# Kernel optimization log

Hardware: AMD Instinct MI355X
Metric: run time of the kernel (lower is better)

## Reference

```python
import jax, jax.numpy as jnp
import numpy as np

B, N, D, H = 2, 512, 64, 128  # batch, tokens, feature dim, hidden (=2*D)
OUT = 64


def setup_inputs() -> dict:
    key = jax.random.key(0)
    ks = jax.random.split(key, 11)
    sH = 1.0 / np.sqrt(H)
    inp = {
        "x": jax.random.normal(ks[0], (B, N, D), dtype=jnp.float32),
        # inner MLP: Linear(2D->H), ReLU, Linear(H->H), ReLU, Linear(H->H)
        "W1": jax.random.normal(ks[1], (2 * D, H), dtype=jnp.float32) / np.sqrt(2 * D),
        "b1": jnp.zeros((H,), jnp.float32),
        "W2": jax.random.normal(ks[2], (H, H), dtype=jnp.float32) * sH,
        "b2": jnp.zeros((H,), jnp.float32),
        "W3": jax.random.normal(ks[3], (H, H), dtype=jnp.float32) * sH,
        "b3": jnp.zeros((H,), jnp.float32),
        # outer MLP: Linear(H->H), ReLU, Linear(H->OUT)
        "V1": jax.random.normal(ks[4], (H, H), dtype=jnp.float32) * sH,
        "c1": jnp.zeros((H,), jnp.float32),
        "V2": jax.random.normal(ks[5], (H, OUT), dtype=jnp.float32) * sH,
        "c2": jnp.zeros((OUT,), jnp.float32),
    }
    return inp


def reference(x, W1, b1, W2, b2, W3, b3, V1, c1, V2, c2):
    d = x.shape[-1]
    # pair[b,i,j] = cat(x[b,j], x[b,i]); fuse cat with first linear:
    # pair @ W1 = x[b,j] @ W1[:d] + x[b,i] @ W1[d:]
    xa = jnp.einsum('bnd,dh->bnh', x, W1[:d])   # contribution of pair_a (index j)
    xb = jnp.einsum('bnd,dh->bnh', x, W1[d:])   # contribution of pair_b (index i)
    h = jax.nn.relu(xa[:, None, :, :] + xb[:, :, None, :] + b1)  # [B,N,N,H]
    h = jax.nn.relu(jnp.einsum('bijh,hk->bijk', h, W2) + b2)
    rel = jnp.einsum('bijh,hk->bijk', h, W3) + b3                # inner output [B,N,N,H]
    pooled = rel.sum(axis=(1, 2))                                # [B,H]
    o = jax.nn.relu(pooled @ V1 + c1)
    return o @ V2 + c2                                           # [B,OUT]
```

## Files before the change

### kernel.cpp

```cpp
#include <hip/hip_runtime.h>
#include <hip/hip_bf16.h>

#define B_ 2
#define N_ 512
#define D_ 64
#define H_ 128
#define OUT_ 64

using bf16x8 = __attribute__((ext_vector_type(8))) __bf16;
using f32x4  = __attribute__((ext_vector_type(4))) float;


__global__ __launch_bounds__(256) void prep_kernel(
    const float* __restrict__ x, const float* __restrict__ W1,
    const float* __restrict__ b1, const float* __restrict__ W2,
    float* __restrict__ xa, float* __restrict__ xb,
    __hip_bfloat16* __restrict__ w2t, float* __restrict__ S)
{
    int idx = blockIdx.x * 256 + threadIdx.x;
    if (idx < B_ * N_ * H_) {
        int h  = idx & (H_ - 1);
        int bn = idx >> 7;
        const float* xr = x + bn * D_;
        float aa = 0.f, ab = 0.f;
        #pragma unroll
        for (int k = 0; k < D_; k++) {
            float xv = xr[k];
            aa += xv * W1[k * H_ + h];
            ab += xv * W1[(k + D_) * H_ + h];
        }
        xa[idx] = aa + b1[h];
        xb[idx] = ab;
    }
    if (idx < H_ * H_) {
        int k = idx & (H_ - 1);
        int n = idx >> 7;
        w2t[n * H_ + k] = __float2bfloat16(W2[k * H_ + n]);
    }
    if (idx < B_ * H_) S[idx] = 0.f;
}

__global__ __launch_bounds__(256, 2) void pair_kernel(
    const float* __restrict__ xa, const float* __restrict__ xb,
    const uint4* __restrict__ w2t, const float* __restrict__ b2,
    float* __restrict__ S)
{
    const int tid  = threadIdx.x;
    const int lane = tid & 63;
    const int wid  = tid >> 6;
    const int l15  = lane & 15;
    const int quad = lane >> 4;

    const int j0 = blockIdx.x * 16;
    const int i0 = blockIdx.y * 64;
    const int b  = blockIdx.z;

    bf16x8 bfrag[8][4];
    #pragma unroll
    for (int c = 0; c < 8; c++) {
        int row = 16 * c + l15;
        #pragma unroll
        for (int s = 0; s < 4; s++) {
            union { uint4 u; bf16x8 v; } cv;
            cv.u = w2t[row * 16 + s * 4 + quad];
            bfrag[c][s] = cv.v;
        }
    }

    const float* xaB = xa + (size_t)(b * N_ + j0 + l15) * H_;
    f32x4 av[4][2];
    #pragma unroll
    for (int s = 0; s < 4; s++) {
        const f32x4* p = (const f32x4*)(xaB + s * 32 + quad * 8);
        av[s][0] = p[0];
        av[s][1] = p[1];
    }

    float b2v[8];
    #pragma unroll
    for (int c = 0; c < 8; c++) b2v[c] = b2[16 * c + l15];

    float csum[8];
    #pragma unroll
    for (int c = 0; c < 8; c++) csum[c] = 0.f;

    const float* xbB = xb + (size_t)(b * N_) * H_;

    for (int r = 0; r < 16; r++) {
        const int i = i0 + wid * 16 + r;
        const float* xr = xbB + i * H_;

        bf16x8 afr[4];
        #pragma unroll
        for (int s = 0; s < 4; s++) {
            const f32x4* p = (const f32x4*)(xr + s * 32 + quad * 8);
            f32x4 u0 = p[0], u1 = p[1];
            f32x4 v0 = av[s][0], v1 = av[s][1];
            bf16x8 a;
            #pragma unroll
            for (int t = 0; t < 4; t++) {
                float f0 = v0[t] + u0[t]; f0 = f0 > 0.f ? f0 : 0.f;
                float f1 = v1[t] + u1[t]; f1 = f1 > 0.f ? f1 : 0.f;
                a[t]     = (__bf16)f0;
                a[t + 4] = (__bf16)f1;
            }
            afr[s] = a;
        }

        #pragma unroll
        for (int c = 0; c < 8; c++) {
            f32x4 acc = {0.f, 0.f, 0.f, 0.f};
            #pragma unroll
            for (int s = 0; s < 4; s++)
                acc = __builtin_amdgcn_mfma_f32_16x16x32_bf16(afr[s], bfrag[c][s], acc, 0, 0, 0);
            float t0 = acc[0] + b2v[c]; t0 = t0 > 0.f ? t0 : 0.f;
            float t1 = acc[1] + b2v[c]; t1 = t1 > 0.f ? t1 : 0.f;
            float t2 = acc[2] + b2v[c]; t2 = t2 > 0.f ? t2 : 0.f;
            float t3 = acc[3] + b2v[c]; t3 = t3 > 0.f ? t3 : 0.f;
            csum[c] += t0 + t1 + t2 + t3;
        }
    }

    #pragma unroll
    for (int c = 0; c < 8; c++) {
        float v = csum[c];
        v += __shfl_xor(v, 16, 64);
        v += __shfl_xor(v, 32, 64);
        csum[c] = v;
    }

    __shared__ float sred[4][H_];
    if (lane < 16) {
        #pragma unroll
        for (int c = 0; c < 8; c++) sred[wid][c * 16 + l15] = csum[c];
    }
    __syncthreads();
    if (tid < H_) {
        float tot = sred[0][tid] + sred[1][tid] + sred[2][tid] + sred[3][tid];
        atomicAdd(&S[b * H_ + tid], tot);
    }
}

__global__ __launch_bounds__(128) void tail_kernel(
    const float* __restrict__ S, const float* __restrict__ W3,
    const float* __restrict__ b3, const float* __restrict__ V1,
    const float* __restrict__ c1, const float* __restrict__ V2,
    const float* __restrict__ c2, float* __restrict__ out)
{
    __shared__ float pool[H_], ov[H_];
    const int b = blockIdx.x, t = threadIdx.x;
    const float* Sb = S + b * H_;
    float acc = 0.f;
    for (int k = 0; k < H_; k++) acc += Sb[k] * W3[k * H_ + t];
    pool[t] = acc + (float)(N_ * N_) * b3[t];
    __syncthreads();
    acc = c1[t];
    for (int k = 0; k < H_; k++) acc += pool[k] * V1[k * H_ + t];
    ov[t] = acc > 0.f ? acc : 0.f;
    __syncthreads();
    if (t < OUT_) {
        acc = c2[t];
        for (int k = 0; k < H_; k++) acc += ov[k] * V2[k * OUT_ + t];
        out[b * OUT_ + t] = acc;
    }
}

extern "C" void kernel_launch(void* const* d_in, const int* in_sizes, int n_in,
                              void* d_out, int out_size, void* d_ws, size_t ws_size,
                              hipStream_t stream) {
    const float* x  = (const float*)d_in[0];
    const float* W1 = (const float*)d_in[1];
    const float* b1 = (const float*)d_in[2];
    const float* W2 = (const float*)d_in[3];
    const float* b2 = (const float*)d_in[4];
    const float* W3 = (const float*)d_in[5];
    const float* b3 = (const float*)d_in[6];
    const float* V1 = (const float*)d_in[7];
    const float* c1 = (const float*)d_in[8];
    const float* V2 = (const float*)d_in[9];
    const float* c2 = (const float*)d_in[10];
    float* out = (float*)d_out;

    char* ws = (char*)d_ws;
    float*          xa  = (float*)(ws);
    float*          xb  = (float*)(ws + 524288);
    __hip_bfloat16* w2t = (__hip_bfloat16*)(ws + 1048576);
    float*          S   = (float*)(ws + 1048576 + 32768);

    prep_kernel<<<512, 256, 0, stream>>>(x, W1, b1, W2, xa, xb, w2t, S);
    dim3 g2(N_ / 16, N_ / 64, B_);
    pair_kernel<<<g2, 256, 0, stream>>>(xa, xb, (const uint4*)w2t, b2, S);
    tail_kernel<<<B_, 128, 0, stream>>>(S, W3, b3, V1, c1, V2, c2, out);
}
```

Measured before the change: 119.8 us.

## Restructure prep with shared-memory x, double pair grid, vectorize pair inner loop

The prep kernel now stages two x rows per block in shared memory and uses split accumulators, and folds the W2 transpose into 32 threads per block. The pair kernel processes 32 rows of i per block instead of 64, doubling the grid so more CUs are busy, and it fully unrolls the row loop. The add/ReLU/bf16 conversion and the bias/ReLU accumulation are vectorised, which defers the per-lane reduction. Doubling the grid also doubles the per-block reloads of W2 fragments and xa, and doubles the atomic adds.

```diff
diff --git a/kernel.cpp b/kernel.cpp
--- a/kernel.cpp
+++ b/kernel.cpp
@@ -9,6 +9,7 @@
 
 using bf16x8 = __attribute__((ext_vector_type(8))) __bf16;
 using f32x4  = __attribute__((ext_vector_type(4))) float;
+using f32x8  = __attribute__((ext_vector_type(8))) float;
 
 
 __global__ __launch_bounds__(256) void prep_kernel(
@@ -17,27 +18,35 @@
     float* __restrict__ xa, float* __restrict__ xb,
     __hip_bfloat16* __restrict__ w2t, float* __restrict__ S)
 {
-    int idx = blockIdx.x * 256 + threadIdx.x;
-    if (idx < B_ * N_ * H_) {
-        int h  = idx & (H_ - 1);
-        int bn = idx >> 7;
-        const float* xr = x + bn * D_;
-        float aa = 0.f, ab = 0.f;
-        #pragma unroll
-        for (int k = 0; k < D_; k++) {
-            float xv = xr[k];
-            aa += xv * W1[k * H_ + h];
-            ab += xv * W1[(k + D_) * H_ + h];
-        }
-        xa[idx] = aa + b1[h];
-        xb[idx] = ab;
-    }
-    if (idx < H_ * H_) {
-        int k = idx & (H_ - 1);
-        int n = idx >> 7;
+    const int tid = threadIdx.x;
+    const int blk = blockIdx.x;
+    __shared__ float xs[128];
+    if (tid < 128) xs[tid] = x[blk * 128 + tid];
+    if (tid < 32) {
+        int e = blk * 32 + tid;
+        int k = e & (H_ - 1), n = e >> 7;
         w2t[n * H_ + k] = __float2bfloat16(W2[k * H_ + n]);
     }
-    if (idx < B_ * H_) S[idx] = 0.f;
+    if (blk == 0) S[tid] = 0.f;
+    __syncthreads();
+
+    const int h = tid & (H_ - 1);
+    const int which = tid >> 7;
+    const float* xr = xs + which * D_;
+    const float* Wa = W1 + h;
+    const float* Wb = W1 + D_ * H_ + h;
+    float a0 = 0.f, a1 = 0.f, p0 = 0.f, p1 = 0.f;
+    #pragma unroll 8
+    for (int k = 0; k < D_; k += 2) {
+        float x0 = xr[k], x1 = xr[k + 1];
+        a0 += x0 * Wa[k * H_];
+        a1 += x1 * Wa[(k + 1) * H_];
+        p0 += x0 * Wb[k * H_];
+        p1 += x1 * Wb[(k + 1) * H_];
+    }
+    const int bn = blk * 2 + which;
+    xa[bn * H_ + h] = a0 + a1 + b1[h];
+    xb[bn * H_ + h] = p0 + p1;
 }
 
 __global__ __launch_bounds__(256, 2) void pair_kernel(
@@ -52,7 +61,7 @@
     const int quad = lane >> 4;
 
     const int j0 = blockIdx.x * 16;
-    const int i0 = blockIdx.y * 64;
+    const int i0 = blockIdx.y * 32;
     const int b  = blockIdx.z;
 
     bf16x8 bfrag[8][4];
@@ -67,72 +76,51 @@
         }
     }
 
-    const float* xaB = xa + (size_t)(b * N_ + j0 + l15) * H_;
-    f32x4 av[4][2];
+    const float* xaB = xa + (size_t)(b * N_ + j0 + l15) * H_ + quad * 8;
+    f32x8 av[4];
     #pragma unroll
-    for (int s = 0; s < 4; s++) {
-        const f32x4* p = (const f32x4*)(xaB + s * 32 + quad * 8);
-        av[s][0] = p[0];
-        av[s][1] = p[1];
-    }
+    for (int s = 0; s < 4; s++) av[s] = *(const f32x8*)(xaB + s * 32);
 
-    float b2v[8];
+    float b2s[8];
     #pragma unroll
-    for (int c = 0; c < 8; c++) b2v[c] = b2[16 * c + l15];
+    for (int c = 0; c < 8; c++) b2s[c] = b2[16 * c + l15];
 
-    float csum[8];
+    f32x4 csum[8];
     #pragma unroll
-    for (int c = 0; c < 8; c++) csum[c] = 0.f;
+    for (int c = 0; c < 8; c++) csum[c] = (f32x4)0.f;
 
-    const float* xbB = xb + (size_t)(b * N_) * H_;
+    const float* xbB = xb + (size_t)(b * N_ + i0 + wid * 8) * H_ + quad * 8;
 
-    for (int r = 0; r < 16; r++) {
-        const int i = i0 + wid * 16 + r;
-        const float* xr = xbB + i * H_;
-
+    #pragma unroll
+    for (int r = 0; r < 8; r++) {
+        const float* xr = xbB + r * H_;
         bf16x8 afr[4];
         #pragma unroll
         for (int s = 0; s < 4; s++) {
-            const f32x4* p = (const f32x4*)(xr + s * 32 + quad * 8);
-            f32x4 u0 = p[0], u1 = p[1];
-            f32x4 v0 = av[s][0], v1 = av[s][1];
-            bf16x8 a;
-            #pragma unroll
-            for (int t = 0; t < 4; t++) {
-                float f0 = v0[t] + u0[t]; f0 = f0 > 0.f ? f0 : 0.f;
-                float f1 = v1[t] + u1[t]; f1 = f1 > 0.f ? f1 : 0.f;
-                a[t]     = (__bf16)f0;
-                a[t + 4] = (__bf16)f1;
-            }
-            afr[s] = a;
+            f32x8 u = *(const f32x8*)(xr + s * 32);
+            f32x8 v = av[s] + u;
+            v = __builtin_elementwise_max(v, (f32x8)0.f);
+            afr[s] = __builtin_convertvector(v, bf16x8);
         }
-
         #pragma unroll
         for (int c = 0; c < 8; c++) {
-            f32x4 acc = {0.f, 0.f, 0.f, 0.f};
+            f32x4 acc = (f32x4)0.f;
             #pragma unroll
             for (int s = 0; s < 4; s++)
                 acc = __builtin_amdgcn_mfma_f32_16x16x32_bf16(afr[s], bfrag[c][s], acc, 0, 0, 0);
-            float t0 = acc[0] + b2v[c]; t0 = t0 > 0.f ? t0 : 0.f;
-            float t1 = acc[1] + b2v[c]; t1 = t1 > 0.f ? t1 : 0.f;
-            float t2 = acc[2] + b2v[c]; t2 = t2 > 0.f ? t2 : 0.f;
-            float t3 = acc[3] + b2v[c]; t3 = t3 > 0.f ? t3 : 0.f;
-            csum[c] += t0 + t1 + t2 + t3;
+            f32x4 t = acc + b2s[c];
+            t = __builtin_elementwise_max(t, (f32x4)0.f);
+            csum[c] += t;
         }
     }
 
+    __shared__ float sred[4][H_];
     #pragma unroll
     for (int c = 0; c < 8; c++) {
-        float v = csum[c];
+        float v = (csum[c][0] + csum[c][1]) + (csum[c][2] + csum[c][3]);
         v += __shfl_xor(v, 16, 64);
         v += __shfl_xor(v, 32, 64);
-        csum[c] = v;
-    }
-
-    __shared__ float sred[4][H_];
-    if (lane < 16) {
-        #pragma unroll
-        for (int c = 0; c < 8; c++) sred[wid][c * 16 + l15] = csum[c];
+        if (quad == 0) sred[wid][c * 16 + l15] = v;
     }
     __syncthreads();
     if (tid < H_) {
@@ -151,15 +139,18 @@
     const int b = blockIdx.x, t = threadIdx.x;
     const float* Sb = S + b * H_;
     float acc = 0.f;
+    #pragma unroll 8
     for (int k = 0; k < H_; k++) acc += Sb[k] * W3[k * H_ + t];
     pool[t] = acc + (float)(N_ * N_) * b3[t];
     __syncthreads();
     acc = c1[t];
+    #pragma unroll 8
     for (int k = 0; k < H_; k++) acc += pool[k] * V1[k * H_ + t];
     ov[t] = acc > 0.f ? acc : 0.f;
     __syncthreads();
     if (t < OUT_) {
         acc = c2[t];
+        #pragma unroll 8
         for (int k = 0; k < H_; k++) acc += ov[k] * V2[k * OUT_ + t];
         out[b * OUT_ + t] = acc;
     }
@@ -187,8 +178,8 @@
     __hip_bfloat16* w2t = (__hip_bfloat16*)(ws + 1048576);
     float*          S   = (float*)(ws + 1048576 + 32768);
 
-    prep_kernel<<<512, 256, 0, stream>>>(x, W1, b1, W2, xa, xb, w2t, S);
-    dim3 g2(N_ / 16, N_ / 64, B_);
+    prep_kernel<<<B_ * N_ / 2, 256, 0, stream>>>(x, W1, b1, W2, xa, xb, w2t, S);
+    dim3 g2(N_ / 16, N_ / 32, B_);
     pair_kernel<<<g2, 256, 0, stream>>>(xa, xb, (const uint4*)w2t, b2, S);
     tail_kernel<<<B_, 128, 0, stream>>>(S, W3, b3, V1, c1, V2, c2, out);
 }
```

Measured after the change: 224.7 us. 87.6% more time.
